# Kernel optimization log

Measured on AMD Instinct MI355X. Metric: run time of the kernel, lower is better.

## Reference

```python
import jax, jax.numpy as jnp
import numpy as np

MU_DT = 0.01
INIT_STD = 0.05

# hidden layers use tanh; last layer is identity (utils.Linear())

def setup_inputs() -> dict:
    key = jax.random.key(0)
    ks = jax.random.split(key, 7)
    B = 512
    nodes = [1024, 4096, 4096, 3072]
    img_batch = jax.random.normal(ks[0], (B, nodes[3]), dtype=jnp.float32)
    mu0 = INIT_STD * jax.random.normal(ks[1], (B, nodes[0]), dtype=jnp.float32)
    mu1 = INIT_STD * jax.random.normal(ks[2], (B, nodes[1]), dtype=jnp.float32)
    mu2 = INIT_STD * jax.random.normal(ks[3], (B, nodes[2]), dtype=jnp.float32)
    W0 = jax.random.normal(ks[4], (nodes[0], nodes[1]), dtype=jnp.float32) / jnp.sqrt(jnp.float32(nodes[0]))
    W1 = jax.random.normal(ks[5], (nodes[1], nodes[2]), dtype=jnp.float32) / jnp.sqrt(jnp.float32(nodes[1]))
    W2 = jax.random.normal(ks[6], (nodes[2], nodes[3]), dtype=jnp.float32) / jnp.sqrt(jnp.float32(nodes[2]))
    return {"img_batch": img_batch, "mu0": mu0, "mu1": mu1, "mu2": mu2,
            "W0": W0, "W1": W1, "W2": W2, "n_iters": 20}


def reference(img_batch, mu0, mu1, mu2, W0, W1, W2, n_iters):
    Ws = (W0, W1, W2)
    L = 3  # n_layers
    acts = (jnp.tanh, jnp.tanh, lambda h: h)
    dacts = (lambda h: 1.0 - jnp.tanh(h) ** 2,
             lambda h: 1.0 - jnp.tanh(h) ** 2,
             lambda h: jnp.ones_like(h))

    def preds_errs(mus):
        # preds[0] = 0, so errs[0] = mus[0]
        hs, errs = [], [mus[0]]
        for l in range(L):
            h = mus[l] @ Ws[l]          # [B, nodes[l+1]]
            hs.append(h)
            errs.append(mus[l + 1] - acts[l](h))
        return hs, errs

    def body(mus, _):
        # prediction pass with current mus (matches stored layer inputs/errs)
        hs, errs = preds_errs(mus)
        new_mus = []
        for l in range(L):
            back = (errs[l + 1] * dacts[l](hs[l])) @ Ws[l].T
            new_mus.append(mus[l] + MU_DT * (back - errs[l]))
        new_mus.append(mus[L])  # target clamped
        return tuple(new_mus), None

    mus = (mu0, mu1, mu2, img_batch)
    mus, _ = jax.lax.scan(body, mus, None, length=n_iters)
    # final prediction/error pass (end of last torch iteration)
    _, errs = preds_errs(mus)
    return jnp.concatenate(errs, axis=1)  # [B, 1024+4096+4096+3072]
```

## Files before the change

### kernel.cpp

```cpp
#include <hip/hip_runtime.h>
#include <hip/hip_bf16.h>
#include <hip/hip_fp8.h>
#include <stdint.h>

typedef __hip_bfloat16 bf16_t;
typedef __attribute__((ext_vector_type(8))) short bf16x8;
typedef __attribute__((ext_vector_type(4))) float f32x4;

#define MU_DT 0.01f
#define S8 8.0f
#define INV_S64 (1.0f / 64.0f)

__device__ inline uint8_t f2fp8(float x) {
  __hip_fp8_e4m3 t(x);
  return t.__x;
}

__device__ inline void gload_lds16(const void* g, void* lds) {
  __builtin_amdgcn_global_load_lds((const __attribute__((address_space(1))) void*)g,
                                   (__attribute__((address_space(3))) void*)lds, 16, 0, 0);
}

struct Seg { int start, layer, tmBase, tilesN; };

struct GemmLayer8 {
  const uint8_t* A;
  const uint8_t* Bt;
  const float*  X;
  const float*  E;
  float*        O1;
  uint8_t*      O2a;
  bf16_t*       O2b;
  int K, N, mode;
};
struct GemmArgs8 { GemmLayer8 L[3]; Seg seg[8]; };

__global__ __launch_bounds__(512) void gemm_fp8(GemmArgs8 args) {
  __shared__ __align__(16) uint8_t As[2 * 64 * 128];
  __shared__ __align__(16) uint8_t Bs[2 * 128 * 128];

  const int bid = blockIdx.x;
  int s = 0;
#pragma unroll
  for (int i = 1; i < 8; ++i)
    if (bid >= args.seg[i].start) s = i;
  const Seg sg = args.seg[s];
  const GemmLayer8 Lr = args.L[sg.layer];
  const int local = bid - sg.start;
  const int tm = sg.tmBase + local / sg.tilesN;
  const int tn = local % sg.tilesN;
  const int K = Lr.K;
  const int rowBase = tm * 64;
  const int colBase = tn * 128;

  const int tid  = threadIdx.x;
  const int lane = tid & 63;
  const int wv   = tid >> 6;
  const int wrM  = wv >> 2;
  const int wcN  = wv & 3;
  const int lo   = lane & 15, hi = lane >> 4;

  f32x4 acc[2][2];
#pragma unroll
  for (int m = 0; m < 2; ++m)
#pragma unroll
    for (int n = 0; n < 2; ++n)
      acc[m][n] = f32x4{0.f, 0.f, 0.f, 0.f};

  char* AsB = (char*)As;
  char* BsB = (char*)Bs;

  const uint8_t* pA0;
  const uint8_t* pB[2];
  {
    const int c = tid;
    const int r = c >> 3, sw = (c & 7) ^ (r & 7);
    pA0 = Lr.A + (size_t)(rowBase + r) * K + sw * 16;
  }
#pragma unroll
  for (int j = 0; j < 2; ++j) {
    const int c = j * 512 + tid;
    const int r = c >> 3, sw = (c & 7) ^ (r & 7);
    pB[j] = Lr.Bt + (size_t)(colBase + r) * K + sw * 16;
  }

  int aoff[2][4], boff[2][4];
#pragma unroll
  for (int m = 0; m < 2; ++m) {
    const int row = wrM * 32 + m * 16 + lo;
#pragma unroll
    for (int kk = 0; kk < 4; ++kk)
      aoff[m][kk] = row * 128 + (((kk * 2 + (hi >> 1)) ^ (row & 7)) << 4) + ((hi & 1) << 3);
  }
#pragma unroll
  for (int n = 0; n < 2; ++n) {
    const int row = wcN * 32 + n * 16 + lo;
#pragma unroll
    for (int kk = 0; kk < 4; ++kk)
      boff[n][kk] = row * 128 + (((kk * 2 + (hi >> 1)) ^ (row & 7)) << 4) + ((hi & 1) << 3);
  }

  const int waveB = wv * 1024;
  const int nkt = K >> 7;

  gload_lds16(pA0,   AsB + waveB);
  gload_lds16(pB[0], BsB + waveB);
  gload_lds16(pB[1], BsB + 8192 + waveB);
  __syncthreads();

  int cur = 0;
  for (int kt = 0; kt < nkt; ++kt) {
    const int curA = cur * 8192, curB = cur * 16384;
    if (kt + 1 < nkt) {
      const int ke = (kt + 1) * 128;
      gload_lds16(pA0 + ke,   AsB + (curA ^ 8192) + waveB);
      gload_lds16(pB[0] + ke, BsB + (curB ^ 16384) + waveB);
      gload_lds16(pB[1] + ke, BsB + (curB ^ 16384) + 8192 + waveB);
    }

    long a[2][4], b[2][4];
#pragma unroll
    for (int m = 0; m < 2; ++m)
#pragma unroll
      for (int kk = 0; kk < 4; ++kk)
        a[m][kk] = *(const long*)(AsB + curA + aoff[m][kk]);
#pragma unroll
    for (int n = 0; n < 2; ++n)
#pragma unroll
      for (int kk = 0; kk < 4; ++kk)
        b[n][kk] = *(const long*)(BsB + curB + boff[n][kk]);

#pragma unroll
    for (int kk = 0; kk < 4; ++kk)
#pragma unroll
      for (int m = 0; m < 2; ++m)
#pragma unroll
        for (int n = 0; n < 2; ++n)
          acc[m][n] = __builtin_amdgcn_mfma_f32_16x16x32_fp8_fp8(a[m][kk], b[n][kk], acc[m][n], 0, 0, 0);

    if (kt + 1 < nkt) {
      __syncthreads();
      cur ^= 1;
    }
  }

  const int N = Lr.N;
#pragma unroll
  for (int m = 0; m < 2; ++m) {
#pragma unroll
    for (int n = 0; n < 2; ++n) {
#pragma unroll
      for (int r = 0; r < 4; ++r) {
        const int row = rowBase + wrM * 32 + m * 16 + hi * 4 + r;
        const int col = colBase + wcN * 32 + n * 16 + lo;
        const float v = acc[m][n][r] * INV_S64;
        const size_t iN = (size_t)row * N + col;
        if (Lr.mode == 0) {
          const float mu = Lr.X[iN];
          const float t  = tanhf(v);
          const float e  = mu - t;
          Lr.O1[iN]  = e;
          Lr.O2a[iN] = f2fp8(e * (1.0f - t * t) * S8);
        } else if (Lr.mode == 1) {
          const float e = Lr.X[iN] - v;
          Lr.O1[iN]  = e;
          Lr.O2a[iN] = f2fp8(e * S8);
        } else {
          const float mu = Lr.X[iN];
          const float sub = (Lr.mode == 2) ? mu : Lr.E[iN];
          const float nv = mu + MU_DT * (v - sub);
          Lr.O1[iN]  = nv;
          Lr.O2a[iN] = f2fp8(nv * S8);
          Lr.O2b[iN] = __float2bfloat16(nv);
        }
      }
    }
  }
}

struct GemmLayer {
  const bf16_t* A;
  const bf16_t* Bt;
  const float*  X;
  const float*  E;
  float*        O1;
  bf16_t*       O2;
  int K, N, ostride, mode;
};
struct GemmArgs { GemmLayer L[3]; Seg seg[8]; };

__global__ __launch_bounds__(512) void gemm_bf16(GemmArgs args) {
  __shared__ __align__(16) bf16_t As[2 * 64 * 64];
  __shared__ __align__(16) bf16_t Bs[2 * 128 * 64];

  const int bid = blockIdx.x;
  int s = 0;
#pragma unroll
  for (int i = 1; i < 8; ++i)
    if (bid >= args.seg[i].start) s = i;
  const Seg sg = args.seg[s];
  const GemmLayer Lr = args.L[sg.layer];
  const int local = bid - sg.start;
  const int tm = sg.tmBase + local / sg.tilesN;
  const int tn = local % sg.tilesN;
  const int K = Lr.K;
  const int rowBase = tm * 64;
  const int colBase = tn * 128;

  const int tid  = threadIdx.x;
  const int lane = tid & 63;
  const int wv   = tid >> 6;
  const int wrM  = wv >> 2;
  const int wcN  = wv & 3;
  const int lo   = lane & 15, hi = lane >> 4;

  f32x4 acc[2][2];
#pragma unroll
  for (int m = 0; m < 2; ++m)
#pragma unroll
    for (int n = 0; n < 2; ++n)
      acc[m][n] = f32x4{0.f, 0.f, 0.f, 0.f};

  char* AsB = (char*)As;
  char* BsB = (char*)Bs;

  const bf16_t* pA0;
  const bf16_t* pB[2];
  {
    const int c = tid;
    const int r = c >> 3, sw = (c & 7) ^ (r & 7);
    pA0 = Lr.A + (size_t)(rowBase + r) * K + sw * 8;
  }
#pragma unroll
  for (int j = 0; j < 2; ++j) {
    const int c = j * 512 + tid;
    const int r = c >> 3, sw = (c & 7) ^ (r & 7);
    pB[j] = Lr.Bt + (size_t)(colBase + r) * K + sw * 8;
  }

  int aoff[2][2], boff[2][2];
#pragma unroll
  for (int m = 0; m < 2; ++m) {
    const int row = wrM * 32 + m * 16 + lo;
#pragma unroll
    for (int kk = 0; kk < 2; ++kk)
      aoff[m][kk] = row * 128 + (((kk * 4 + hi) ^ (row & 7)) << 4);
  }
#pragma unroll
  for (int n = 0; n < 2; ++n) {
    const int row = wcN * 32 + n * 16 + lo;
#pragma unroll
    for (int kk = 0; kk < 2; ++kk)
      boff[n][kk] = row * 128 + (((kk * 4 + hi) ^ (row & 7)) << 4);
  }

  const int waveB = wv * 1024;
  const int nkt = K >> 6;

  gload_lds16(pA0,   AsB + waveB);
  gload_lds16(pB[0], BsB + waveB);
  gload_lds16(pB[1], BsB + 8192 + waveB);
  __syncthreads();

  int cur = 0;
  for (int kt = 0; kt < nkt; ++kt) {
    const int curA = cur * 8192, curB = cur * 16384;
    if (kt + 1 < nkt) {
      const int ke = (kt + 1) * 64;
      gload_lds16(pA0 + ke,   AsB + (curA ^ 8192) + waveB);
      gload_lds16(pB[0] + ke, BsB + (curB ^ 16384) + waveB);
      gload_lds16(pB[1] + ke, BsB + (curB ^ 16384) + 8192 + waveB);
    }

    bf16x8 a[2][2], b[2][2];
#pragma unroll
    for (int m = 0; m < 2; ++m)
#pragma unroll
      for (int kk = 0; kk < 2; ++kk)
        a[m][kk] = *(const bf16x8*)(AsB + curA + aoff[m][kk]);
#pragma unroll
    for (int n = 0; n < 2; ++n)
#pragma unroll
      for (int kk = 0; kk < 2; ++kk)
        b[n][kk] = *(const bf16x8*)(BsB + curB + boff[n][kk]);

#pragma unroll
    for (int kk = 0; kk < 2; ++kk)
#pragma unroll
      for (int m = 0; m < 2; ++m)
#pragma unroll
        for (int n = 0; n < 2; ++n)
          acc[m][n] = __builtin_amdgcn_mfma_f32_16x16x32_bf16(a[m][kk], b[n][kk], acc[m][n], 0, 0, 0);

    if (kt + 1 < nkt) {
      __syncthreads();
      cur ^= 1;
    }
  }

  const int N = Lr.N;
#pragma unroll
  for (int m = 0; m < 2; ++m) {
#pragma unroll
    for (int n = 0; n < 2; ++n) {
#pragma unroll
      for (int r = 0; r < 4; ++r) {
        const int row = rowBase + wrM * 32 + m * 16 + hi * 4 + r;
        const int col = colBase + wcN * 32 + n * 16 + lo;
        const float v = acc[m][n][r];
        const size_t iN = (size_t)row * N + col;
        const size_t iO = (size_t)row * Lr.ostride + col;
        if (Lr.mode == 0) {
          const float mu = Lr.X[iN];
          const float t  = tanhf(v);
          const float e  = mu - t;
          Lr.O1[iO] = e;
          Lr.O2[iN] = __float2bfloat16(e * (1.0f - t * t));
        } else if (Lr.mode == 1) {
          const float e = Lr.X[iN] - v;
          Lr.O1[iO] = e;
          Lr.O2[iN] = __float2bfloat16(e);
        }
      }
    }
  }
}

__global__ void prep_all(const float* __restrict__ W, bf16_t* __restrict__ WTb,
                         uint8_t* __restrict__ W8, uint8_t* __restrict__ WT8,
                         int R, int C) {
  __shared__ float t[64][65];
  const int tx = threadIdx.x, ty = threadIdx.y;
  const int c0 = blockIdx.x * 64, r0 = blockIdx.y * 64;
  for (int rr = ty; rr < 64; rr += 4) {
    const float v = W[(size_t)(r0 + rr) * C + c0 + tx];
    W8[(size_t)(r0 + rr) * C + c0 + tx] = f2fp8(v * S8);
    t[rr][tx] = v;
  }
  __syncthreads();
  for (int rr = ty; rr < 64; rr += 4) {
    const float v = t[tx][rr];
    WTb[(size_t)(c0 + rr) * R + r0 + tx] = __float2bfloat16(v);
    WT8[(size_t)(c0 + rr) * R + r0 + tx] = f2fp8(v * S8);
  }
}

__global__ void copy_cast3(const float* __restrict__ in, float* __restrict__ of,
                           uint8_t* __restrict__ o8, bf16_t* __restrict__ ob, int n) {
  const int i = blockIdx.x * blockDim.x + threadIdx.x;
  if (i < n) {
    const float v = in[i];
    of[i] = v;
    o8[i] = f2fp8(v * S8);
    ob[i] = __float2bfloat16(v);
  }
}

__global__ void copy_e0(const float* __restrict__ mu0, float* __restrict__ out) {
  const int i = blockIdx.x * blockDim.x + threadIdx.x;
  if (i < 512 * 1024) {
    const int b = i >> 10, j = i & 1023;
    out[(size_t)b * 12288 + j] = mu0[i];
  }
}

extern "C" void kernel_launch(void* const* d_in, const int* in_sizes, int n_in,
                              void* d_out, int out_size, void* d_ws, size_t ws_size,
                              hipStream_t stream) {
  const float* img  = (const float*)d_in[0];
  const float* mu0i = (const float*)d_in[1];
  const float* mu1i = (const float*)d_in[2];
  const float* mu2i = (const float*)d_in[3];
  const float* W0   = (const float*)d_in[4];
  const float* W1   = (const float*)d_in[5];
  const float* W2   = (const float*)d_in[6];
  float* out = (float*)d_out;
  const int n_iters = 20;

  char* p = (char*)d_ws;
  auto alloc = [&](size_t bytes) -> char* {
    char* r = p;
    p += (bytes + 255) & ~(size_t)255;
    return r;
  };
  bf16_t* WT0 = (bf16_t*)alloc((size_t)4096 * 1024 * 2);
  bf16_t* WT1 = (bf16_t*)alloc((size_t)4096 * 4096 * 2);
  bf16_t* WT2 = (bf16_t*)alloc((size_t)3072 * 4096 * 2);
  uint8_t* W80  = (uint8_t*)alloc((size_t)1024 * 4096);
  uint8_t* W81  = (uint8_t*)alloc((size_t)4096 * 4096);
  uint8_t* W82  = (uint8_t*)alloc((size_t)4096 * 3072);
  uint8_t* WT80 = (uint8_t*)alloc((size_t)4096 * 1024);
  uint8_t* WT81 = (uint8_t*)alloc((size_t)4096 * 4096);
  uint8_t* WT82 = (uint8_t*)alloc((size_t)3072 * 4096);
  float*   mu0 = (float*)alloc((size_t)512 * 1024 * 4);
  float*   mu1 = (float*)alloc((size_t)512 * 4096 * 4);
  float*   mu2 = (float*)alloc((size_t)512 * 4096 * 4);
  uint8_t* m80 = (uint8_t*)alloc((size_t)512 * 1024);
  uint8_t* m81 = (uint8_t*)alloc((size_t)512 * 4096);
  uint8_t* m82 = (uint8_t*)alloc((size_t)512 * 4096);
  bf16_t*  mb0 = (bf16_t*)alloc((size_t)512 * 1024 * 2);
  bf16_t*  mb1 = (bf16_t*)alloc((size_t)512 * 4096 * 2);
  bf16_t*  mb2 = (bf16_t*)alloc((size_t)512 * 4096 * 2);
  float*   e1  = (float*)alloc((size_t)512 * 4096 * 4);
  float*   e2  = (float*)alloc((size_t)512 * 4096 * 4);
  float*   e3  = (float*)alloc((size_t)512 * 3072 * 4);
  uint8_t* G80 = (uint8_t*)alloc((size_t)512 * 4096);
  uint8_t* G81 = (uint8_t*)alloc((size_t)512 * 4096);
  uint8_t* G82 = (uint8_t*)alloc((size_t)512 * 3072);
  bf16_t*  Gb0 = (bf16_t*)alloc((size_t)512 * 4096 * 2);
  bf16_t*  Gb1 = (bf16_t*)alloc((size_t)512 * 4096 * 2);
  bf16_t*  Gb2 = (bf16_t*)alloc((size_t)512 * 3072 * 2);
  (void)ws_size;

  dim3 tb(64, 4);
  prep_all<<<dim3(4096 / 64, 1024 / 64), tb, 0, stream>>>(W0, WT0, W80, WT80, 1024, 4096);
  prep_all<<<dim3(4096 / 64, 4096 / 64), tb, 0, stream>>>(W1, WT1, W81, WT81, 4096, 4096);
  prep_all<<<dim3(3072 / 64, 4096 / 64), tb, 0, stream>>>(W2, WT2, W82, WT82, 4096, 3072);
  copy_cast3<<<(512 * 1024 + 255) / 256, 256, 0, stream>>>(mu0i, mu0, m80, mb0, 512 * 1024);
  copy_cast3<<<(512 * 4096 + 255) / 256, 256, 0, stream>>>(mu1i, mu1, m81, mb1, 512 * 4096);
  copy_cast3<<<(512 * 4096 + 255) / 256, 256, 0, stream>>>(mu2i, mu2, m82, mb2, 512 * 4096);

  const Seg SENT = { 1 << 30, 0, 0, 1 };

  GemmArgs8 fa;
  fa.L[0] = { m80, WT80, mu1, nullptr, e1, G80, nullptr, 1024, 4096, 0 };
  fa.L[1] = { m81, WT81, mu2, nullptr, e2, G81, nullptr, 4096, 4096, 0 };
  fa.L[2] = { m82, WT82, img, nullptr, e3, G82, nullptr, 4096, 3072, 1 };
  fa.seg[0] = { 0,   0, 0, 32 };
  fa.seg[1] = { 256, 1, 0, 32 };
  fa.seg[2] = { 512, 2, 0, 24 };
  fa.seg[3] = SENT; fa.seg[4] = SENT; fa.seg[5] = SENT;
  fa.seg[6] = SENT; fa.seg[7] = SENT;
  const int fwdBlocks = 704;

  GemmArgs8 ba;
  ba.L[0] = { G80, W80, mu0, nullptr, mu0, m80, mb0, 4096, 1024, 2 };
  ba.L[1] = { G81, W81, mu1, e1,      mu1, m81, mb1, 4096, 4096, 3 };
  ba.L[2] = { G82, W82, mu2, e2,      mu2, m82, mb2, 3072, 4096, 3 };
  ba.seg[0] = { 0,   2, 0, 32 };
  ba.seg[1] = { 64,  1, 0, 32 };
  ba.seg[2] = { 192, 2, 6, 32 };
  ba.seg[3] = { 256, 2, 2, 32 };
  ba.seg[4] = { 320, 1, 4, 32 };
  ba.seg[5] = { 448, 0, 0, 8 };
  ba.seg[6] = { 512, 2, 4, 32 };
  ba.seg[7] = SENT;
  const int bwdBlocks = 576;

  GemmArgs faF;
  faF.L[0] = { mb0, WT0, mu1, nullptr, out + 1024, Gb0, 1024, 4096, 12288, 0 };
  faF.L[1] = { mb1, WT1, mu2, nullptr, out + 5120, Gb1, 4096, 4096, 12288, 0 };
  faF.L[2] = { mb2, WT2, img, nullptr, out + 9216, Gb2, 4096, 3072, 12288, 1 };
  faF.seg[0] = { 0,   0, 0, 32 };
  faF.seg[1] = { 256, 1, 0, 32 };
  faF.seg[2] = { 512, 2, 0, 24 };
  faF.seg[3] = SENT; faF.seg[4] = SENT; faF.seg[5] = SENT;
  faF.seg[6] = SENT; faF.seg[7] = SENT;

  for (int it = 0; it < n_iters; ++it) {
    gemm_fp8<<<fwdBlocks, 512, 0, stream>>>(fa);
    gemm_fp8<<<bwdBlocks, 512, 0, stream>>>(ba);
  }
  gemm_bf16<<<fwdBlocks, 512, 0, stream>>>(faF);
  copy_e0<<<(512 * 1024 + 255) / 256, 256, 0, stream>>>(mu0, out);
}
```

Measured before the change: 2.222 ms.

## Enlarge fp8 GEMM tile to 128x128 with 1024-thread blocks

The fp8 GEMM block tile grows from 64x128 to 128x128 and blocks go from 512 to 1024 threads (16 waves, still 32x32 per wave). A and B tiles are each loaded with one 16-byte global-to-LDS copy per thread. Block counts are halved and the segment tables for the forward and backward launches are reorganised to match. The goal is to cut redundant global and L2 traffic for the weight operand through more reuse per block, at the cost of fewer blocks (288 in the backward launch), which risks poorer CU balance and tail effects.

```diff
diff --git a/kernel.cpp b/kernel.cpp
--- a/kernel.cpp
+++ b/kernel.cpp
@@ -35,8 +35,8 @@
 };
 struct GemmArgs8 { GemmLayer8 L[3]; Seg seg[8]; };
 
-__global__ __launch_bounds__(512) void gemm_fp8(GemmArgs8 args) {
-  __shared__ __align__(16) uint8_t As[2 * 64 * 128];
+__global__ __launch_bounds__(1024) void gemm_fp8(GemmArgs8 args) {
+  __shared__ __align__(16) uint8_t As[2 * 128 * 128];
   __shared__ __align__(16) uint8_t Bs[2 * 128 * 128];
 
   const int bid = blockIdx.x;
@@ -50,7 +50,7 @@
   const int tm = sg.tmBase + local / sg.tilesN;
   const int tn = local % sg.tilesN;
   const int K = Lr.K;
-  const int rowBase = tm * 64;
+  const int rowBase = tm * 128;
   const int colBase = tn * 128;
 
   const int tid  = threadIdx.x;
@@ -71,17 +71,12 @@
   char* BsB = (char*)Bs;
 
   const uint8_t* pA0;
-  const uint8_t* pB[2];
+  const uint8_t* pB0;
   {
     const int c = tid;
     const int r = c >> 3, sw = (c & 7) ^ (r & 7);
-    pA0 = Lr.A + (size_t)(rowBase + r) * K + sw * 16;
-  }
-#pragma unroll
-  for (int j = 0; j < 2; ++j) {
-    const int c = j * 512 + tid;
-    const int r = c >> 3, sw = (c & 7) ^ (r & 7);
-    pB[j] = Lr.Bt + (size_t)(colBase + r) * K + sw * 16;
+    pA0 = Lr.A  + (size_t)(rowBase + r) * K + sw * 16;
+    pB0 = Lr.Bt + (size_t)(colBase + r) * K + sw * 16;
   }
 
   int aoff[2][4], boff[2][4];
@@ -103,19 +98,17 @@
   const int waveB = wv * 1024;
   const int nkt = K >> 7;
 
-  gload_lds16(pA0,   AsB + waveB);
-  gload_lds16(pB[0], BsB + waveB);
-  gload_lds16(pB[1], BsB + 8192 + waveB);
+  gload_lds16(pA0, AsB + waveB);
+  gload_lds16(pB0, BsB + waveB);
   __syncthreads();
 
   int cur = 0;
   for (int kt = 0; kt < nkt; ++kt) {
-    const int curA = cur * 8192, curB = cur * 16384;
+    const int curO = cur * 16384;
     if (kt + 1 < nkt) {
       const int ke = (kt + 1) * 128;
-      gload_lds16(pA0 + ke,   AsB + (curA ^ 8192) + waveB);
-      gload_lds16(pB[0] + ke, BsB + (curB ^ 16384) + waveB);
-      gload_lds16(pB[1] + ke, BsB + (curB ^ 16384) + 8192 + waveB);
+      gload_lds16(pA0 + ke, AsB + (curO ^ 16384) + waveB);
+      gload_lds16(pB0 + ke, BsB + (curO ^ 16384) + waveB);
     }
 
     long a[2][4], b[2][4];
@@ -123,12 +116,12 @@
     for (int m = 0; m < 2; ++m)
 #pragma unroll
       for (int kk = 0; kk < 4; ++kk)
-        a[m][kk] = *(const long*)(AsB + curA + aoff[m][kk]);
+        a[m][kk] = *(const long*)(AsB + curO + aoff[m][kk]);
 #pragma unroll
     for (int n = 0; n < 2; ++n)
 #pragma unroll
       for (int kk = 0; kk < 4; ++kk)
-        b[n][kk] = *(const long*)(BsB + curB + boff[n][kk]);
+        b[n][kk] = *(const long*)(BsB + curO + boff[n][kk]);
 
 #pragma unroll
     for (int kk = 0; kk < 4; ++kk)
@@ -426,26 +419,24 @@
   fa.L[0] = { m80, WT80, mu1, nullptr, e1, G80, nullptr, 1024, 4096, 0 };
   fa.L[1] = { m81, WT81, mu2, nullptr, e2, G81, nullptr, 4096, 4096, 0 };
   fa.L[2] = { m82, WT82, img, nullptr, e3, G82, nullptr, 4096, 3072, 1 };
-  fa.seg[0] = { 0,   0, 0, 32 };
-  fa.seg[1] = { 256, 1, 0, 32 };
-  fa.seg[2] = { 512, 2, 0, 24 };
-  fa.seg[3] = SENT; fa.seg[4] = SENT; fa.seg[5] = SENT;
-  fa.seg[6] = SENT; fa.seg[7] = SENT;
-  const int fwdBlocks = 704;
+  fa.seg[0] = { 0,   2, 0, 24 };
+  fa.seg[1] = { 96,  1, 0, 32 };
+  fa.seg[2] = { 224, 0, 0, 32 };
+  fa.seg[3] = { 256, 0, 1, 32 };
+  fa.seg[4] = SENT; fa.seg[5] = SENT; fa.seg[6] = SENT; fa.seg[7] = SENT;
+  const int fwdBlocks = 352;
 
   GemmArgs8 ba;
   ba.L[0] = { G80, W80, mu0, nullptr, mu0, m80, mb0, 4096, 1024, 2 };
   ba.L[1] = { G81, W81, mu1, e1,      mu1, m81, mb1, 4096, 4096, 3 };
   ba.L[2] = { G82, W82, mu2, e2,      mu2, m82, mb2, 3072, 4096, 3 };
   ba.seg[0] = { 0,   2, 0, 32 };
-  ba.seg[1] = { 64,  1, 0, 32 };
-  ba.seg[2] = { 192, 2, 6, 32 };
-  ba.seg[3] = { 256, 2, 2, 32 };
-  ba.seg[4] = { 320, 1, 4, 32 };
-  ba.seg[5] = { 448, 0, 0, 8 };
-  ba.seg[6] = { 512, 2, 4, 32 };
-  ba.seg[7] = SENT;
-  const int bwdBlocks = 576;
+  ba.seg[1] = { 32,  1, 0, 32 };
+  ba.seg[2] = { 160, 0, 0, 8 };
+  ba.seg[3] = { 192, 2, 1, 32 };
+  ba.seg[4] = { 256, 2, 3, 32 };
+  ba.seg[5] = SENT; ba.seg[6] = SENT; ba.seg[7] = SENT;
+  const int bwdBlocks = 288;
 
   GemmArgs faF;
   faF.L[0] = { mb0, WT0, mu1, nullptr, out + 1024, Gb0, 1024, 4096, 12288, 0 };
@@ -458,9 +449,9 @@
   faF.seg[6] = SENT; faF.seg[7] = SENT;
 
   for (int it = 0; it < n_iters; ++it) {
-    gemm_fp8<<<fwdBlocks, 512, 0, stream>>>(fa);
-    gemm_fp8<<<bwdBlocks, 512, 0, stream>>>(ba);
-  }
-  gemm_bf16<<<fwdBlocks, 512, 0, stream>>>(faF);
+    gemm_fp8<<<fwdBlocks, 1024, 0, stream>>>(fa);
+    gemm_fp8<<<bwdBlocks, 1024, 0, stream>>>(ba);
+  }
+  gemm_bf16<<<704, 512, 0, stream>>>(faF);
   copy_e0<<<(512 * 1024 + 255) / 256, 256, 0, stream>>>(mu0, out);
 }
```

After: 2.596 ms. 1.17x slower.

## Loop multiple output tiles per block for small forward layer; drop unused final outputs

Applied to the files above, without the earlier changes.

Adds an nSub field so a block can compute several N-tiles in sequence. The forward fp8 pass now assigns each of the 64 layer-0 (K=1024) blocks four column tiles, which cuts the grid from 704 to 512 blocks so it fits one wave of work per CU and the short-K tiles ride along with the long-K ones. The final bf16 pass also stops writing the unused bf16 gradient buffers and frees them. The cost is a longer tail for the layer-0 blocks, which now run four serial K=1024 GEMM tiles, plus an extra sync between tiles.

```diff
diff --git a/kernel.cpp b/kernel.cpp
--- a/kernel.cpp
+++ b/kernel.cpp
@@ -21,7 +21,7 @@
                                    (__attribute__((address_space(3))) void*)lds, 16, 0, 0);
 }
 
-struct Seg { int start, layer, tmBase, tilesN; };
+struct Seg { int start, layer, tmBase, tilesN, nSub; };
 
 struct GemmLayer8 {
   const uint8_t* A;
@@ -48,10 +48,9 @@
   const GemmLayer8 Lr = args.L[sg.layer];
   const int local = bid - sg.start;
   const int tm = sg.tmBase + local / sg.tilesN;
-  const int tn = local % sg.tilesN;
+  const int tn0 = local % sg.tilesN;
   const int K = Lr.K;
   const int rowBase = tm * 64;
-  const int colBase = tn * 128;
 
   const int tid  = threadIdx.x;
   const int lane = tid & 63;
@@ -60,30 +59,15 @@
   const int wcN  = wv & 3;
   const int lo   = lane & 15, hi = lane >> 4;
 
-  f32x4 acc[2][2];
-#pragma unroll
-  for (int m = 0; m < 2; ++m)
-#pragma unroll
-    for (int n = 0; n < 2; ++n)
-      acc[m][n] = f32x4{0.f, 0.f, 0.f, 0.f};
-
   char* AsB = (char*)As;
   char* BsB = (char*)Bs;
 
   const uint8_t* pA0;
-  const uint8_t* pB[2];
   {
     const int c = tid;
     const int r = c >> 3, sw = (c & 7) ^ (r & 7);
     pA0 = Lr.A + (size_t)(rowBase + r) * K + sw * 16;
   }
-#pragma unroll
-  for (int j = 0; j < 2; ++j) {
-    const int c = j * 512 + tid;
-    const int r = c >> 3, sw = (c & 7) ^ (r & 7);
-    pB[j] = Lr.Bt + (size_t)(colBase + r) * K + sw * 16;
-  }
-
   int aoff[2][4], boff[2][4];
 #pragma unroll
   for (int m = 0; m < 2; ++m) {
@@ -103,75 +87,96 @@
   const int waveB = wv * 1024;
   const int nkt = K >> 7;
 
-  gload_lds16(pA0,   AsB + waveB);
-  gload_lds16(pB[0], BsB + waveB);
-  gload_lds16(pB[1], BsB + 8192 + waveB);
-  __syncthreads();
-
-  int cur = 0;
-  for (int kt = 0; kt < nkt; ++kt) {
-    const int curA = cur * 8192, curB = cur * 16384;
-    if (kt + 1 < nkt) {
-      const int ke = (kt + 1) * 128;
-      gload_lds16(pA0 + ke,   AsB + (curA ^ 8192) + waveB);
-      gload_lds16(pB[0] + ke, BsB + (curB ^ 16384) + waveB);
-      gload_lds16(pB[1] + ke, BsB + (curB ^ 16384) + 8192 + waveB);
-    }
-
-    long a[2][4], b[2][4];
+  for (int sub = 0; sub < sg.nSub; ++sub) {
+    if (sub) __syncthreads();
+    const int tn = tn0 + sub * sg.tilesN;
+    const int colBase = tn * 128;
+
+    const uint8_t* pB[2];
+#pragma unroll
+    for (int j = 0; j < 2; ++j) {
+      const int c = j * 512 + tid;
+      const int r = c >> 3, sw = (c & 7) ^ (r & 7);
+      pB[j] = Lr.Bt + (size_t)(colBase + r) * K + sw * 16;
+    }
+
+    f32x4 acc[2][2];
 #pragma unroll
     for (int m = 0; m < 2; ++m)
 #pragma unroll
+      for (int n = 0; n < 2; ++n)
+        acc[m][n] = f32x4{0.f, 0.f, 0.f, 0.f};
+
+    gload_lds16(pA0,   AsB + waveB);
+    gload_lds16(pB[0], BsB + waveB);
+    gload_lds16(pB[1], BsB + 8192 + waveB);
+    __syncthreads();
+
+    int cur = 0;
+    for (int kt = 0; kt < nkt; ++kt) {
+      const int curA = cur * 8192, curB = cur * 16384;
+      if (kt + 1 < nkt) {
+        const int ke = (kt + 1) * 128;
+        gload_lds16(pA0 + ke,   AsB + (curA ^ 8192) + waveB);
+        gload_lds16(pB[0] + ke, BsB + (curB ^ 16384) + waveB);
+        gload_lds16(pB[1] + ke, BsB + (curB ^ 16384) + 8192 + waveB);
+      }
+
+      long a[2][4], b[2][4];
+#pragma unroll
+      for (int m = 0; m < 2; ++m)
+#pragma unroll
+        for (int kk = 0; kk < 4; ++kk)
+          a[m][kk] = *(const long*)(AsB + curA + aoff[m][kk]);
+#pragma unroll
+      for (int n = 0; n < 2; ++n)
+#pragma unroll
+        for (int kk = 0; kk < 4; ++kk)
+          b[n][kk] = *(const long*)(BsB + curB + boff[n][kk]);
+
+#pragma unroll
       for (int kk = 0; kk < 4; ++kk)
-        a[m][kk] = *(const long*)(AsB + curA + aoff[m][kk]);
-#pragma unroll
-    for (int n = 0; n < 2; ++n)
-#pragma unroll
-      for (int kk = 0; kk < 4; ++kk)
-        b[n][kk] = *(const long*)(BsB + curB + boff[n][kk]);
-
-#pragma unroll
-    for (int kk = 0; kk < 4; ++kk)
-#pragma unroll
-      for (int m = 0; m < 2; ++m)
-#pragma unroll
-        for (int n = 0; n < 2; ++n)
-          acc[m][n] = __builtin_amdgcn_mfma_f32_16x16x32_fp8_fp8(a[m][kk], b[n][kk], acc[m][n], 0, 0, 0);
-
-    if (kt + 1 < nkt) {
-      __syncthreads();
-      cur ^= 1;
-    }
-  }
-
-  const int N = Lr.N;
-#pragma unroll
-  for (int m = 0; m < 2; ++m) {
-#pragma unroll
-    for (int n = 0; n < 2; ++n) {
-#pragma unroll
-      for (int r = 0; r < 4; ++r) {
-        const int row = rowBase + wrM * 32 + m * 16 + hi * 4 + r;
-        const int col = colBase + wcN * 32 + n * 16 + lo;
-        const float v = acc[m][n][r] * INV_S64;
-        const size_t iN = (size_t)row * N + col;
-        if (Lr.mode == 0) {
-          const float mu = Lr.X[iN];
-          const float t  = tanhf(v);
-          const float e  = mu - t;
-          Lr.O1[iN]  = e;
-          Lr.O2a[iN] = f2fp8(e * (1.0f - t * t) * S8);
-        } else if (Lr.mode == 1) {
-          const float e = Lr.X[iN] - v;
-          Lr.O1[iN]  = e;
-          Lr.O2a[iN] = f2fp8(e * S8);
-        } else {
-          const float mu = Lr.X[iN];
-          const float sub = (Lr.mode == 2) ? mu : Lr.E[iN];
-          const float nv = mu + MU_DT * (v - sub);
-          Lr.O1[iN]  = nv;
-          Lr.O2a[iN] = f2fp8(nv * S8);
-          Lr.O2b[iN] = __float2bfloat16(nv);
+#pragma unroll
+        for (int m = 0; m < 2; ++m)
+#pragma unroll
+          for (int n = 0; n < 2; ++n)
+            acc[m][n] = __builtin_amdgcn_mfma_f32_16x16x32_fp8_fp8(a[m][kk], b[n][kk], acc[m][n], 0, 0, 0);
+
+      if (kt + 1 < nkt) {
+        __syncthreads();
+        cur ^= 1;
+      }
+    }
+
+    const int N = Lr.N;
+#pragma unroll
+    for (int m = 0; m < 2; ++m) {
+#pragma unroll
+      for (int n = 0; n < 2; ++n) {
+#pragma unroll
+        for (int r = 0; r < 4; ++r) {
+          const int row = rowBase + wrM * 32 + m * 16 + hi * 4 + r;
+          const int col = colBase + wcN * 32 + n * 16 + lo;
+          const float v = acc[m][n][r] * INV_S64;
+          const size_t iN = (size_t)row * N + col;
+          if (Lr.mode == 0) {
+            const float mu = Lr.X[iN];
+            const float t  = tanhf(v);
+            const float e  = mu - t;
+            Lr.O1[iN]  = e;
+            Lr.O2a[iN] = f2fp8(e * (1.0f - t * t) * S8);
+          } else if (Lr.mode == 1) {
+            const float e = Lr.X[iN] - v;
+            Lr.O1[iN]  = e;
+            Lr.O2a[iN] = f2fp8(e * S8);
+          } else {
+            const float mu = Lr.X[iN];
+            const float sub2 = (Lr.mode == 2) ? mu : Lr.E[iN];
+            const float nv = mu + MU_DT * (v - sub2);
+            Lr.O1[iN]  = nv;
+            Lr.O2a[iN] = f2fp8(nv * S8);
+            Lr.O2b[iN] = __float2bfloat16(nv);
+          }
         }
       }
     }
@@ -182,9 +187,7 @@
   const bf16_t* A;
   const bf16_t* Bt;
   const float*  X;
-  const float*  E;
   float*        O1;
-  bf16_t*       O2;
   int K, N, ostride, mode;
 };
 struct GemmArgs { GemmLayer L[3]; Seg seg[8]; };
@@ -311,15 +314,9 @@
         const size_t iN = (size_t)row * N + col;
         const size_t iO = (size_t)row * Lr.ostride + col;
         if (Lr.mode == 0) {
-          const float mu = Lr.X[iN];
-          const float t  = tanhf(v);
-          const float e  = mu - t;
-          Lr.O1[iO] = e;
-          Lr.O2[iN] = __float2bfloat16(e * (1.0f - t * t));
-        } else if (Lr.mode == 1) {
-          const float e = Lr.X[iN] - v;
-          Lr.O1[iO] = e;
-          Lr.O2[iN] = __float2bfloat16(e);
+          Lr.O1[iO] = Lr.X[iN] - tanhf(v);
+        } else {
+          Lr.O1[iO] = Lr.X[iN] - v;
         }
       }
     }
@@ -407,9 +404,6 @@
   uint8_t* G80 = (uint8_t*)alloc((size_t)512 * 4096);
   uint8_t* G81 = (uint8_t*)alloc((size_t)512 * 4096);
   uint8_t* G82 = (uint8_t*)alloc((size_t)512 * 3072);
-  bf16_t*  Gb0 = (bf16_t*)alloc((size_t)512 * 4096 * 2);
-  bf16_t*  Gb1 = (bf16_t*)alloc((size_t)512 * 4096 * 2);
-  bf16_t*  Gb2 = (bf16_t*)alloc((size_t)512 * 3072 * 2);
   (void)ws_size;
 
   dim3 tb(64, 4);
@@ -420,40 +414,40 @@
   copy_cast3<<<(512 * 4096 + 255) / 256, 256, 0, stream>>>(mu1i, mu1, m81, mb1, 512 * 4096);
   copy_cast3<<<(512 * 4096 + 255) / 256, 256, 0, stream>>>(mu2i, mu2, m82, mb2, 512 * 4096);
 
-  const Seg SENT = { 1 << 30, 0, 0, 1 };
+  const Seg SENT = { 1 << 30, 0, 0, 1, 1 };
 
   GemmArgs8 fa;
   fa.L[0] = { m80, WT80, mu1, nullptr, e1, G80, nullptr, 1024, 4096, 0 };
   fa.L[1] = { m81, WT81, mu2, nullptr, e2, G81, nullptr, 4096, 4096, 0 };
   fa.L[2] = { m82, WT82, img, nullptr, e3, G82, nullptr, 4096, 3072, 1 };
-  fa.seg[0] = { 0,   0, 0, 32 };
-  fa.seg[1] = { 256, 1, 0, 32 };
-  fa.seg[2] = { 512, 2, 0, 24 };
+  fa.seg[0] = { 0,   1, 0, 32, 1 };
+  fa.seg[1] = { 256, 2, 0, 24, 1 };
+  fa.seg[2] = { 448, 0, 0, 8,  4 };
   fa.seg[3] = SENT; fa.seg[4] = SENT; fa.seg[5] = SENT;
   fa.seg[6] = SENT; fa.seg[7] = SENT;
-  const int fwdBlocks = 704;
+  const int fwdBlocks = 512;
 
   GemmArgs8 ba;
   ba.L[0] = { G80, W80, mu0, nullptr, mu0, m80, mb0, 4096, 1024, 2 };
   ba.L[1] = { G81, W81, mu1, e1,      mu1, m81, mb1, 4096, 4096, 3 };
   ba.L[2] = { G82, W82, mu2, e2,      mu2, m82, mb2, 3072, 4096, 3 };
-  ba.seg[0] = { 0,   2, 0, 32 };
-  ba.seg[1] = { 64,  1, 0, 32 };
-  ba.seg[2] = { 192, 2, 6, 32 };
-  ba.seg[3] = { 256, 2, 2, 32 };
-  ba.seg[4] = { 320, 1, 4, 32 };
-  ba.seg[5] = { 448, 0, 0, 8 };
-  ba.seg[6] = { 512, 2, 4, 32 };
+  ba.seg[0] = { 0,   2, 0, 32, 1 };
+  ba.seg[1] = { 64,  1, 0, 32, 1 };
+  ba.seg[2] = { 192, 2, 6, 32, 1 };
+  ba.seg[3] = { 256, 2, 2, 32, 1 };
+  ba.seg[4] = { 320, 1, 4, 32, 1 };
+  ba.seg[5] = { 448, 0, 0, 8,  1 };
+  ba.seg[6] = { 512, 2, 4, 32, 1 };
   ba.seg[7] = SENT;
   const int bwdBlocks = 576;
 
   GemmArgs faF;
-  faF.L[0] = { mb0, WT0, mu1, nullptr, out + 1024, Gb0, 1024, 4096, 12288, 0 };
-  faF.L[1] = { mb1, WT1, mu2, nullptr, out + 5120, Gb1, 4096, 4096, 12288, 0 };
-  faF.L[2] = { mb2, WT2, img, nullptr, out + 9216, Gb2, 4096, 3072, 12288, 1 };
-  faF.seg[0] = { 0,   0, 0, 32 };
-  faF.seg[1] = { 256, 1, 0, 32 };
-  faF.seg[2] = { 512, 2, 0, 24 };
+  faF.L[0] = { mb0, WT0, mu1, out + 1024, 1024, 4096, 12288, 0 };
+  faF.L[1] = { mb1, WT1, mu2, out + 5120, 4096, 4096, 12288, 0 };
+  faF.L[2] = { mb2, WT2, img, out + 9216, 4096, 3072, 12288, 1 };
+  faF.seg[0] = { 0,   0, 0, 32, 1 };
+  faF.seg[1] = { 256, 1, 0, 32, 1 };
+  faF.seg[2] = { 512, 2, 0, 24, 1 };
   faF.seg[3] = SENT; faF.seg[4] = SENT; faF.seg[5] = SENT;
   faF.seg[6] = SENT; faF.seg[7] = SENT;
 
@@ -461,6 +455,6 @@
     gemm_fp8<<<fwdBlocks, 512, 0, stream>>>(fa);
     gemm_fp8<<<bwdBlocks, 512, 0, stream>>>(ba);
   }
-  gemm_bf16<<<fwdBlocks, 512, 0, stream>>>(faF);
+  gemm_bf16<<<704, 512, 0, stream>>>(faF);
   copy_e0<<<(512 * 1024 + 255) / 256, 256, 0, stream>>>(mu0, out);
 }
```

Result: slower. 2.812 ms (+26.5%).
